# Kernel tuning notes

Measured on AMD Instinct MI355X. Metric: run time of the kernel, lower is better.

## Reference

```python
import jax, jax.numpy as jnp
import numpy as np

N, D_IN, D_OUT, C = 4096, 512, 16384, 256
THRESHOLD = 0.01
TEMPERATURE = 0.1


def setup_inputs() -> dict:
    key = jax.random.key(0)
    k1, k2, k3, k4, k5 = jax.random.split(key, 5)
    inp = jax.random.normal(k1, (N, D_IN), dtype=jnp.float32)
    # kaiming_uniform(a=sqrt(5)) ~ U(-1/sqrt(fan_in), 1/sqrt(fan_in)) scale
    bound = 1.0 / np.sqrt(D_IN)
    weight = jax.random.uniform(k2, (D_OUT, D_IN), minval=-bound, maxval=bound, dtype=jnp.float32)
    bias = jax.random.uniform(k3, (D_OUT,), minval=-bound, maxval=bound, dtype=jnp.float32)
    centroids = jax.random.normal(k4, (C, D_IN), dtype=jnp.float32) * bound
    # disjoint partition of output rows into clusters (stand-in for kmeans labels)
    assignment = jax.random.randint(k5, (D_OUT,), 0, C, dtype=jnp.int32)
    return {"input": inp, "weight": weight, "bias": bias,
            "centroids": centroids, "assignment": assignment}


def reference(input, weight, bias, centroids, assignment):
    # routing: softmax over centroid similarities, threshold
    dots = jax.nn.softmax((input @ centroids.T) / TEMPERATURE, axis=-1)  # [N, C]
    active = dots > THRESHOLD                                            # [N, C] bool
    # torch.unique(query_indices) -> queries active for ANY cluster
    qmask = jnp.any(active, axis=1)                                      # [N]
    # torch.unique(cluster_indices) -> clusters active for ANY query (global union)
    cmask = jnp.any(active, axis=0)                                      # [C]
    # concat(unpad(indices[top_clusters])) -> output rows in any active cluster
    row_mask = cmask[assignment]                                         # [D_OUT]
    # out[top_q].index_copy(1, top_rows, linear(...)); rest stays zero
    dense = input @ weight.T + bias                                      # [N, D_OUT]
    out = dense * qmask[:, None].astype(dense.dtype) * row_mask[None, :].astype(dense.dtype)
    return out
```

## Files before the change

### kernel.cpp

```cpp
#include <hip/hip_runtime.h>
#include <stdint.h>

#define N_Q    4096
#define D_K    512
#define D_OUT  16384
#define NCLUST 256

#define BM 256
#define BN 128
#define BK 32
#define NT (D_K / BK)
#define SCP 132

typedef __attribute__((ext_vector_type(4))) float f32x4;
typedef __attribute__((ext_vector_type(8))) short bf16x8;

__device__ __forceinline__ uint32_t f2bf(float f) {
  uint32_t u = __float_as_uint(f);
  u += 0x7FFFu + ((u >> 16) & 1u);
  return u >> 16;
}

#define GLOAD_LDS16(g, l)                                         \
  __builtin_amdgcn_global_load_lds(                               \
      (const __attribute__((address_space(1))) void*)(g),         \
      (__attribute__((address_space(3))) void*)(l), 16, 0, 0)

#define WAIT_BAR(N) asm volatile("s_waitcnt vmcnt(" #N ")\n\ts_barrier" ::: "memory")
#define LBAR() asm volatile("s_waitcnt lgkmcnt(0)\n\ts_barrier" ::: "memory")

__global__ __launch_bounds__(256) void prep_kernel(const float* __restrict__ weight,
                                                   ushort* __restrict__ W_bf,
                                                   const float* __restrict__ cent,
                                                   float4* __restrict__ centT4,
                                                   float* __restrict__ cmask) {
  int b = blockIdx.x;
  if (b < (D_OUT * D_K / 8) / 256) {
    int i = b * 256 + threadIdx.x;
    const float4* s = reinterpret_cast<const float4*>(weight) + (size_t)i * 2;
    float4 v0 = s[0], v1 = s[1];
    uint4 o;
    o.x = f2bf(v0.x) | (f2bf(v0.y) << 16);
    o.y = f2bf(v0.z) | (f2bf(v0.w) << 16);
    o.z = f2bf(v1.x) | (f2bf(v1.y) << 16);
    o.w = f2bf(v1.z) | (f2bf(v1.w) << 16);
    reinterpret_cast<uint4*>(W_bf)[i] = o;
  } else {
    int bb = b - (D_OUT * D_K / 8) / 256;
    if (bb == 0) cmask[threadIdx.x] = 0.0f;
    int idx = bb * 256 + threadIdx.x;
    int k4 = idx & 127, c = idx >> 7;
    float4 v = *reinterpret_cast<const float4*>(&cent[(size_t)c * D_K + k4 * 4]);
    centT4[(size_t)k4 * NCLUST + c] = v;
  }
}

__global__ __launch_bounds__(256) void routing_kernel(const float* __restrict__ input,
                                                      const float4* __restrict__ centT4,
                                                      float* __restrict__ qmask,
                                                      float* __restrict__ cmask,
                                                      ushort* __restrict__ A_bf) {
  __shared__ float lgs[8][NCLUST];
  int c = threadIdx.x;
  int q0 = blockIdx.x * 8;
  const float* __restrict__ inp = input + (size_t)q0 * D_K;

  {
    const float4* s4 = reinterpret_cast<const float4*>(inp) + c * 4;
    float4 x0 = s4[0], x1 = s4[1], x2 = s4[2], x3 = s4[3];
    uint4 o0, o1;
    o0.x = f2bf(x0.x) | (f2bf(x0.y) << 16);
    o0.y = f2bf(x0.z) | (f2bf(x0.w) << 16);
    o0.z = f2bf(x1.x) | (f2bf(x1.y) << 16);
    o0.w = f2bf(x1.z) | (f2bf(x1.w) << 16);
    o1.x = f2bf(x2.x) | (f2bf(x2.y) << 16);
    o1.y = f2bf(x2.z) | (f2bf(x2.w) << 16);
    o1.z = f2bf(x3.x) | (f2bf(x3.y) << 16);
    o1.w = f2bf(x3.z) | (f2bf(x3.w) << 16);
    uint4* dst = reinterpret_cast<uint4*>(A_bf + (size_t)q0 * D_K);
    dst[c * 2] = o0;
    dst[c * 2 + 1] = o1;
  }

  float acc[8] = {0, 0, 0, 0, 0, 0, 0, 0};
  for (int k4 = 0; k4 < D_K / 4; ++k4) {
    float4 v = centT4[(size_t)k4 * NCLUST + c];
#pragma unroll
    for (int q = 0; q < 8; ++q) {
      float4 r = *reinterpret_cast<const float4*>(&inp[q * D_K + k4 * 4]);
      acc[q] += v.x * r.x + v.y * r.y + v.z * r.z + v.w * r.w;
    }
  }
#pragma unroll
  for (int q = 0; q < 8; ++q) lgs[q][c] = acc[q] * 10.0f;
  __syncthreads();

  int wave = c >> 6, lane = c & 63;
#pragma unroll
  for (int qq = 0; qq < 2; ++qq) {
    int q = wave * 2 + qq;
    float4 lv = *reinterpret_cast<const float4*>(&lgs[q][lane * 4]);
    float m = fmaxf(fmaxf(lv.x, lv.y), fmaxf(lv.z, lv.w));
#pragma unroll
    for (int off = 32; off > 0; off >>= 1) m = fmaxf(m, __shfl_xor(m, off));
    float e0 = expf(lv.x - m), e1 = expf(lv.y - m), e2 = expf(lv.z - m), e3 = expf(lv.w - m);
    float s = e0 + e1 + e2 + e3;
#pragma unroll
    for (int off = 32; off > 0; off >>= 1) s += __shfl_xor(s, off);
    float thr = 0.01f * s;
    bool a0 = e0 > thr, a1 = e1 > thr, a2 = e2 > thr, a3 = e3 > thr;
    if (a0) cmask[lane * 4 + 0] = 1.0f;
    if (a1) cmask[lane * 4 + 1] = 1.0f;
    if (a2) cmask[lane * 4 + 2] = 1.0f;
    if (a3) cmask[lane * 4 + 3] = 1.0f;
    unsigned long long any = __ballot(a0 | a1 | a2 | a3);
    if (lane == 0) qmask[q0 + q] = any ? 1.0f : 0.0f;
  }
}

__global__ __launch_bounds__(256, 2) void gemm_masked_kernel(
    const ushort* __restrict__ A, const ushort* __restrict__ W,
    const float* __restrict__ bias, const int* __restrict__ assign,
    const float* __restrict__ qmask, const float* __restrict__ cmask,
    float* __restrict__ C) {
  __shared__ __align__(16) char smem[73728];

  int tid = threadIdx.x;
  int wave = tid >> 6, lane = tid & 63;

  int bid = blockIdx.x;
  int idx = bid >> 3;
  int ntile = (bid & 7) * 16 + (idx & 15);
  int mtile = idx >> 4;
  int m0 = mtile * BM, n0 = ntile * BN;

  int wr = wave >> 1, wc = wave & 1;

  int srow = tid >> 2, kg = tid & 3;
  int ks = (kg ^ ((srow >> 1) & 3)) * 8;
  const ushort* srcA = A + (size_t)(m0 + srow) * D_K + ks;
  const ushort* srcB = W + (size_t)(n0 + srow) * D_K + ks;
  int wo = wave << 10;

#define STAGE(j) do {                                                    \
    char* sl_ = smem + ((j) % 3) * 24576 + wo;                           \
    GLOAD_LDS16(srcA + (j) * BK, sl_);                                   \
    GLOAD_LDS16(srcA + (size_t)64 * D_K + (j) * BK, sl_ + 4096);         \
    GLOAD_LDS16(srcA + (size_t)128 * D_K + (j) * BK, sl_ + 8192);        \
    GLOAD_LDS16(srcA + (size_t)192 * D_K + (j) * BK, sl_ + 12288);       \
    GLOAD_LDS16(srcB + (j) * BK, sl_ + 16384);                           \
    GLOAD_LDS16(srcB + (size_t)64 * D_K + (j) * BK, sl_ + 20480);        \
  } while (0)

  int kg0 = lane >> 4, l15 = lane & 15, lr = lane >> 4;
  int aIdx[8], bIdx[4];
#pragma unroll
  for (int m = 0; m < 8; ++m) {
    int r = wr * 128 + m * 16 + l15;
    aIdx[m] = r * 32 + ((kg0 ^ ((r >> 1) & 3)) << 3);
  }
#pragma unroll
  for (int n = 0; n < 4; ++n) {
    int r = wc * 64 + n * 16 + l15;
    bIdx[n] = 8192 + r * 32 + ((kg0 ^ ((r >> 1) & 3)) << 3);
  }

  f32x4 acc[8][4] = {};

  STAGE(0);
  STAGE(1);

#pragma unroll
  for (int t = 0; t < NT; ++t) {
    if (t < NT - 1) { WAIT_BAR(6); } else { WAIT_BAR(0); }

    const ushort* sl = (const ushort*)(smem + (t % 3) * 24576);
    bf16x8 af[8], bf[4];
#pragma unroll
    for (int n = 0; n < 4; ++n) bf[n] = *reinterpret_cast<const bf16x8*>(&sl[bIdx[n]]);
#pragma unroll
    for (int m = 0; m < 8; ++m) af[m] = *reinterpret_cast<const bf16x8*>(&sl[aIdx[m]]);
    if (t + 2 < NT) STAGE(t + 2);

    __builtin_amdgcn_s_setprio(1);
#pragma unroll
    for (int m = 0; m < 8; ++m)
#pragma unroll
      for (int n = 0; n < 4; ++n)
        acc[m][n] = __builtin_amdgcn_mfma_f32_16x16x32_bf16(af[m], bf[n], acc[m][n], 0, 0, 0);
    __builtin_amdgcn_s_setprio(0);
  }
#undef STAGE

  LBAR();

  float* sC = reinterpret_cast<float*>(smem);
  float bj[4], rm[4];
#pragma unroll
  for (int n = 0; n < 4; ++n) {
    int col = n0 + wc * 64 + n * 16 + l15;
    bj[n] = bias[col];
    rm[n] = cmask[assign[col]];
  }
#pragma unroll
  for (int s = 0; s < 4; ++s) {
#pragma unroll
    for (int e = 0; e < 2; ++e) {
      int m = 2 * s + e;
      float4 qm = *reinterpret_cast<const float4*>(&qmask[m0 + wr * 128 + m * 16 + lr * 4]);
      int rl = wr * 32 + e * 16 + lr * 4;
#pragma unroll
      for (int n = 0; n < 4; ++n) {
        int cc = wc * 64 + n * 16 + l15;
        sC[(rl + 0) * SCP + cc] = (acc[m][n][0] + bj[n]) * qm.x * rm[n];
        sC[(rl + 1) * SCP + cc] = (acc[m][n][1] + bj[n]) * qm.y * rm[n];
        sC[(rl + 2) * SCP + cc] = (acc[m][n][2] + bj[n]) * qm.z * rm[n];
        sC[(rl + 3) * SCP + cc] = (acc[m][n][3] + bj[n]) * qm.w * rm[n];
      }
    }
    LBAR();
    f32x4 v[8];
#pragma unroll
    for (int i = 0; i < 8; ++i) {
      int rl = wave * 16 + i * 2 + (lane >> 5);
      v[i] = *reinterpret_cast<const f32x4*>(&sC[rl * SCP + (lane & 31) * 4]);
    }
    LBAR();
#pragma unroll
    for (int i = 0; i < 8; ++i) {
      int rl = wave * 16 + i * 2 + (lane >> 5);
      int grow = m0 + (rl >> 5) * 128 + s * 32 + ((rl >> 4) & 1) * 16 + (rl & 15);
      __builtin_nontemporal_store(
          v[i], reinterpret_cast<f32x4*>(&C[(size_t)grow * D_OUT + n0 + (lane & 31) * 4]));
    }
  }
}

extern "C" void kernel_launch(void* const* d_in, const int* in_sizes, int n_in,
                              void* d_out, int out_size, void* d_ws, size_t ws_size,
                              hipStream_t stream) {
  const float* input     = (const float*)d_in[0];
  const float* weight    = (const float*)d_in[1];
  const float* bias      = (const float*)d_in[2];
  const float* centroids = (const float*)d_in[3];
  const int*   assign    = (const int*)d_in[4];
  float* out = (float*)d_out;

  char* ws = (char*)d_ws;
  ushort* A_bf   = (ushort*)ws;
  ushort* W_bf   = (ushort*)(ws + 4194304);
  float*  qmask  = (float*)(ws + 20971520);
  float*  cmask  = (float*)(ws + 20987904);
  float4* centT4 = (float4*)(ws + 21000192);

  prep_kernel<<<4224, 256, 0, stream>>>(weight, W_bf, centroids, centT4, cmask);
  routing_kernel<<<N_Q / 8, 256, 0, stream>>>(input, centT4, qmask, cmask, A_bf);
  gemm_masked_kernel<<<(N_Q / BM) * (D_OUT / BN), 256, 0, stream>>>(
      A_bf, W_bf, bias, assign, qmask, cmask, out);
}
```

Before: 133.0 us.

## Fuse weight bf16 conversion into GEMM B-tile loading via register staging

The separate pass that converts the full fp32 weight matrix to bf16 is removed. The GEMM now loads fp32 weight tiles into registers three stages ahead, converts them with packed bf16 conversion instructions, and writes them swizzled into LDS, while A still uses direct global-to-LDS loads. This avoids writing and re-reading a 16 MB bf16 weight copy and one kernel's worth of work. In exchange each GEMM block reads twice as many bytes for B, re-converts weights once per M tile (16 times), and uses more VGPRs with hand-counted waitcnts.

```diff
diff --git a/kernel.cpp b/kernel.cpp
--- a/kernel.cpp
+++ b/kernel.cpp
@@ -26,33 +26,32 @@
       (const __attribute__((address_space(1))) void*)(g),         \
       (__attribute__((address_space(3))) void*)(l), 16, 0, 0)
 
-#define WAIT_BAR(N) asm volatile("s_waitcnt vmcnt(" #N ")\n\ts_barrier" ::: "memory")
+__device__ __forceinline__ f32x4 gloadf4(const float* p) {
+  f32x4 r;
+  asm volatile("global_load_dwordx4 %0, %1, off" : "=v"(r) : "v"(p));
+  return r;
+}
+__device__ __forceinline__ uint32_t cvtpk(float lo, float hi) {
+  uint32_t r;
+  asm("v_cvt_pk_bf16_f32 %0, %1, %2" : "=v"(r) : "v"(lo), "v"(hi));
+  return r;
+}
+
+#define WAIT_BAR_LG(N) do {                                                     \
+    asm volatile("s_waitcnt vmcnt(" #N ") lgkmcnt(0)\n\ts_barrier" ::: "memory"); \
+    __builtin_amdgcn_sched_barrier(0);                                          \
+  } while (0)
 #define LBAR() asm volatile("s_waitcnt lgkmcnt(0)\n\ts_barrier" ::: "memory")
-
-__global__ __launch_bounds__(256) void prep_kernel(const float* __restrict__ weight,
-                                                   ushort* __restrict__ W_bf,
-                                                   const float* __restrict__ cent,
+#define CFENCE() asm volatile("" ::: "memory")
+
+__global__ __launch_bounds__(256) void cent_kernel(const float* __restrict__ cent,
                                                    float4* __restrict__ centT4,
                                                    float* __restrict__ cmask) {
-  int b = blockIdx.x;
-  if (b < (D_OUT * D_K / 8) / 256) {
-    int i = b * 256 + threadIdx.x;
-    const float4* s = reinterpret_cast<const float4*>(weight) + (size_t)i * 2;
-    float4 v0 = s[0], v1 = s[1];
-    uint4 o;
-    o.x = f2bf(v0.x) | (f2bf(v0.y) << 16);
-    o.y = f2bf(v0.z) | (f2bf(v0.w) << 16);
-    o.z = f2bf(v1.x) | (f2bf(v1.y) << 16);
-    o.w = f2bf(v1.z) | (f2bf(v1.w) << 16);
-    reinterpret_cast<uint4*>(W_bf)[i] = o;
-  } else {
-    int bb = b - (D_OUT * D_K / 8) / 256;
-    if (bb == 0) cmask[threadIdx.x] = 0.0f;
-    int idx = bb * 256 + threadIdx.x;
-    int k4 = idx & 127, c = idx >> 7;
-    float4 v = *reinterpret_cast<const float4*>(&cent[(size_t)c * D_K + k4 * 4]);
-    centT4[(size_t)k4 * NCLUST + c] = v;
-  }
+  if (blockIdx.x == 0) cmask[threadIdx.x] = 0.0f;
+  int idx = blockIdx.x * 256 + threadIdx.x;
+  int k4 = idx & 127, c = idx >> 7;
+  float4 v = *reinterpret_cast<const float4*>(&cent[(size_t)c * D_K + k4 * 4]);
+  centT4[(size_t)k4 * NCLUST + c] = v;
 }
 
 __global__ __launch_bounds__(256) void routing_kernel(const float* __restrict__ input,
@@ -119,7 +118,7 @@
 }
 
 __global__ __launch_bounds__(256, 2) void gemm_masked_kernel(
-    const ushort* __restrict__ A, const ushort* __restrict__ W,
+    const ushort* __restrict__ A, const float* __restrict__ Wf,
     const float* __restrict__ bias, const int* __restrict__ assign,
     const float* __restrict__ qmask, const float* __restrict__ cmask,
     float* __restrict__ C) {
@@ -139,17 +138,35 @@
   int srow = tid >> 2, kg = tid & 3;
   int ks = (kg ^ ((srow >> 1) & 3)) * 8;
   const ushort* srcA = A + (size_t)(m0 + srow) * D_K + ks;
-  const ushort* srcB = W + (size_t)(n0 + srow) * D_K + ks;
   int wo = wave << 10;
 
-#define STAGE(j) do {                                                    \
+#define STAGE_A(j) do {                                                  \
     char* sl_ = smem + ((j) % 3) * 24576 + wo;                           \
     GLOAD_LDS16(srcA + (j) * BK, sl_);                                   \
     GLOAD_LDS16(srcA + (size_t)64 * D_K + (j) * BK, sl_ + 4096);         \
     GLOAD_LDS16(srcA + (size_t)128 * D_K + (j) * BK, sl_ + 8192);        \
     GLOAD_LDS16(srcA + (size_t)192 * D_K + (j) * BK, sl_ + 12288);       \
-    GLOAD_LDS16(srcB + (j) * BK, sl_ + 16384);                           \
-    GLOAD_LDS16(srcB + (size_t)64 * D_K + (j) * BK, sl_ + 20480);        \
+  } while (0)
+
+  int br = tid >> 1, g0 = (tid & 1) * 2;
+  int bswz = (br >> 1) & 3;
+  const float* srcBf = Wf + (size_t)(n0 + br) * D_K + g0 * 8;
+
+#define LOADB(j, d0, d1, d2, d3) do {                    \
+    const float* p_ = srcBf + (j) * BK;                  \
+    d0 = gloadf4(p_); d1 = gloadf4(p_ + 4);              \
+    d2 = gloadf4(p_ + 8); d3 = gloadf4(p_ + 12);         \
+  } while (0)
+
+#define WRITEB(j, d0, d1, d2, d3) do {                                        \
+    char* bb_ = smem + ((j) % 3) * 24576 + 16384 + br * 64;                   \
+    uint4 q0_, q1_;                                                           \
+    q0_.x = cvtpk(d0[0], d0[1]); q0_.y = cvtpk(d0[2], d0[3]);                 \
+    q0_.z = cvtpk(d1[0], d1[1]); q0_.w = cvtpk(d1[2], d1[3]);                 \
+    q1_.x = cvtpk(d2[0], d2[1]); q1_.y = cvtpk(d2[2], d2[3]);                 \
+    q1_.z = cvtpk(d3[0], d3[1]); q1_.w = cvtpk(d3[2], d3[3]);                 \
+    *reinterpret_cast<uint4*>(bb_ + ((g0 ^ bswz) << 4)) = q0_;                \
+    *reinterpret_cast<uint4*>(bb_ + (((g0 + 1) ^ bswz) << 4)) = q1_;          \
   } while (0)
 
   int kg0 = lane >> 4, l15 = lane & 15, lr = lane >> 4;
@@ -167,12 +184,25 @@
 
   f32x4 acc[8][4] = {};
 
-  STAGE(0);
-  STAGE(1);
+  f32x4 b1a, b1b, b1c, b1d, b2a, b2b, b2c, b2d, t0, t1, t2, t3;
+  LOADB(0, b1a, b1b, b1c, b1d);
+  LOADB(1, b2a, b2b, b2c, b2d);
+  LOADB(2, t0, t1, t2, t3);
+  CFENCE();
+  STAGE_A(0);
+  STAGE_A(1);
+  CFENCE();
+  asm volatile("s_waitcnt vmcnt(12)" ::: "memory");
+  WRITEB(0, b1a, b1b, b1c, b1d);
+  b1a = b2a; b1b = b2b; b1c = b2c; b1d = b2d;
+  b2a = t0; b2b = t1; b2c = t2; b2d = t3;
 
 #pragma unroll
   for (int t = 0; t < NT; ++t) {
-    if (t < NT - 1) { WAIT_BAR(6); } else { WAIT_BAR(0); }
+    if (t == 0) { WAIT_BAR_LG(4); }
+    else if (t <= 13) { WAIT_BAR_LG(8); }
+    else if (t == 14) { WAIT_BAR_LG(4); }
+    else { WAIT_BAR_LG(0); }
 
     const ushort* sl = (const ushort*)(smem + (t % 3) * 24576);
     bf16x8 af[8], bf[4];
@@ -180,7 +210,13 @@
     for (int n = 0; n < 4; ++n) bf[n] = *reinterpret_cast<const bf16x8*>(&sl[bIdx[n]]);
 #pragma unroll
     for (int m = 0; m < 8; ++m) af[m] = *reinterpret_cast<const bf16x8*>(&sl[aIdx[m]]);
-    if (t + 2 < NT) STAGE(t + 2);
+
+    if (t + 2 < NT) STAGE_A(t + 2);
+    CFENCE();
+    f32x4 n0r, n1r, n2r, n3r;
+    if (t + 3 < NT) { LOADB(t + 3, n0r, n1r, n2r, n3r); }
+    CFENCE();
+    if (t + 1 < NT) { WRITEB(t + 1, b1a, b1b, b1c, b1d); }
 
     __builtin_amdgcn_s_setprio(1);
 #pragma unroll
@@ -189,8 +225,13 @@
       for (int n = 0; n < 4; ++n)
         acc[m][n] = __builtin_amdgcn_mfma_f32_16x16x32_bf16(af[m], bf[n], acc[m][n], 0, 0, 0);
     __builtin_amdgcn_s_setprio(0);
-  }
-#undef STAGE
+
+    b1a = b2a; b1b = b2b; b1c = b2c; b1d = b2d;
+    if (t + 3 < NT) { b2a = n0r; b2b = n1r; b2c = n2r; b2d = n3r; }
+  }
+#undef STAGE_A
+#undef LOADB
+#undef WRITEB
 
   LBAR();
 
@@ -248,13 +289,12 @@
 
   char* ws = (char*)d_ws;
   ushort* A_bf   = (ushort*)ws;
-  ushort* W_bf   = (ushort*)(ws + 4194304);
   float*  qmask  = (float*)(ws + 20971520);
   float*  cmask  = (float*)(ws + 20987904);
   float4* centT4 = (float4*)(ws + 21000192);
 
-  prep_kernel<<<4224, 256, 0, stream>>>(weight, W_bf, centroids, centT4, cmask);
+  cent_kernel<<<128, 256, 0, stream>>>(centroids, centT4, cmask);
   routing_kernel<<<N_Q / 8, 256, 0, stream>>>(input, centT4, qmask, cmask, A_bf);
   gemm_masked_kernel<<<(N_Q / BM) * (D_OUT / BN), 256, 0, stream>>>(
-      A_bf, W_bf, bias, assign, qmask, cmask, out);
-}
+      A_bf, weight, bias, assign, qmask, cmask, out);
+}
```

New measurement: 157.1 us. 18.1% more time.
